# Kernel tuning notes

Hardware: AMD Instinct MI355X
Metric: run time of the kernel (lower is better)

Reference implementation:

```python
import jax, jax.numpy as jnp
import numpy as np

RES = 128        # 2**base_lod, base_lod=7, num_lod=1
FEAT_DIM = 18


def setup_inputs() -> dict:
    key = jax.random.key(0)
    k1, k2 = jax.random.split(key)
    pts = jax.random.uniform(k1, (4, 524288, 3), dtype=jnp.float32)
    codebook = jax.random.normal(k2, (RES ** 3, FEAT_DIM), dtype=jnp.float32) * 0.01
    transform = jnp.eye(4, dtype=jnp.float32)
    return {"pts": pts, "codebook": codebook, "transform": transform}


def _trilinear(res, codebook, pts):
    # pts: [N,3] in [0,1]; NGLOD-style dense grid trilinear interpolation
    p = pts * (res - 1)
    p0 = jnp.floor(p)
    w = p - p0                                   # [N,3] fractional weights
    i0 = jnp.clip(p0.astype(jnp.int32), 0, res - 1)
    i1 = jnp.clip(i0 + 1, 0, res - 1)
    feats = jnp.zeros((pts.shape[0], codebook.shape[1]), dtype=codebook.dtype)
    for dz in (0, 1):
        iz = (i1 if dz else i0)[:, 2]
        wz = w[:, 2] if dz else 1.0 - w[:, 2]
        for dy in (0, 1):
            iy = (i1 if dy else i0)[:, 1]
            wy = w[:, 1] if dy else 1.0 - w[:, 1]
            for dx in (0, 1):
                ix = (i1 if dx else i0)[:, 0]
                wx = w[:, 0] if dx else 1.0 - w[:, 0]
                idx = ix + iy * res + iz * res * res   # x + y*res + z*res^2
                feats = feats + codebook[idx] * (wx * wy * wz)[:, None]
    return feats


def reference(pts, codebook, transform):
    # flatten 'b h c -> (b h) c'
    p = pts.reshape(-1, 3)
    R_inv = jnp.linalg.inv(transform[:3, :3])
    p = (R_inv @ (p.T - transform[:3, 3:4])).T
    feats = _trilinear(RES, codebook, p)
    # single LOD: cat over lod axis then sum(-1) is identity
    return feats
```

## Files before the change

kernel.cpp:

```cpp
#include <hip/hip_runtime.h>


constexpr int RES  = 128;
constexpr int NBA  = 512;
constexpr int TPM  = 576;
constexpr int PPB  = 64;
constexpr int ROWF = 128 * 18;
constexpr int SUB_CAP = 8160;

constexpr int HIST_CHUNK = 1024;
constexpr int SCAT_CHUNK = 8192;

typedef float vf2 __attribute__((ext_vector_type(2)));
typedef float vf4 __attribute__((ext_vector_type(4)));

struct Xf {
    float m00, m01, m02, m10, m11, m12, m20, m21, m22;
    float tx, ty, tz;
};

__device__ __forceinline__ Xf load_xf(const float* __restrict__ tr) {
    Xf X;
    const float a = tr[0], b = tr[1],  c = tr[2];
    const float d = tr[4], e = tr[5],  g = tr[6];
    const float h = tr[8], i = tr[9],  j = tr[10];
    X.tx = tr[3]; X.ty = tr[7]; X.tz = tr[11];
    const float det = a*(e*j - g*i) - b*(d*j - g*h) + c*(d*i - e*h);
    const float rd  = 1.0f / det;
    X.m00 = (e*j - g*i) * rd; X.m01 = (c*i - b*j) * rd; X.m02 = (b*g - c*e) * rd;
    X.m10 = (g*h - d*j) * rd; X.m11 = (a*j - c*h) * rd; X.m12 = (c*d - a*g) * rd;
    X.m20 = (d*i - e*h) * rd; X.m21 = (b*h - a*i) * rd; X.m22 = (a*e - b*d) * rd;
    return X;
}

__device__ __forceinline__ float qcoord(float m0, float m1, float m2,
                                        float x, float y, float z) {
    return __fmaf_rn(m0, x, __fmaf_rn(m1, y, m2 * z)) * (float)(RES - 1);
}

__device__ __forceinline__ int clamp_idx(float q) {
    return min(max((int)floorf(q), 0), RES - 1);
}

__device__ __forceinline__ int coarse_key(float qy, float qz) {
    return (clamp_idx(qz) << 2) | (clamp_idx(qy) >> 5);
}

__global__ __launch_bounds__(256)
void k_zero(unsigned* __restrict__ histA) {
    const int i = blockIdx.x * 256 + threadIdx.x;
    if (i < NBA) histA[i] = 0u;
}

__global__ __launch_bounds__(256)
void k_histA(const float* __restrict__ pts, const float* __restrict__ tr,
             unsigned* __restrict__ histA, int npts)
{
    __shared__ unsigned sh[NBA];
    const int t = threadIdx.x;
    for (int b = t; b < NBA; b += 256) sh[b] = 0u;
    __syncthreads();
    const Xf X = load_xf(tr);
    const int base = blockIdx.x * HIST_CHUNK;
    #pragma unroll
    for (int i = 0; i < HIST_CHUNK / 256; ++i) {
        const int p = base + t + i * 256;
        if (p < npts) {
            const float x = pts[p*3 + 0] - X.tx;
            const float y = pts[p*3 + 1] - X.ty;
            const float z = pts[p*3 + 2] - X.tz;
            const float qy = qcoord(X.m10, X.m11, X.m12, x, y, z);
            const float qz = qcoord(X.m20, X.m21, X.m22, x, y, z);
            atomicAdd(&sh[coarse_key(qy, qz)], 1u);
        }
    }
    __syncthreads();
    for (int b = t; b < NBA; b += 256) {
        const unsigned c = sh[b];
        if (c) atomicAdd(&histA[b], c);
    }
}

__global__ __launch_bounds__(NBA)
void k_scanA(const unsigned* __restrict__ histA,
             unsigned* __restrict__ baseA, unsigned* __restrict__ cursorA)
{
    __shared__ unsigned s[NBA];
    const int t = threadIdx.x;
    const unsigned my = histA[t];
    s[t] = my;
    __syncthreads();
    for (int off = 1; off < NBA; off <<= 1) {
        const unsigned v = (t >= off) ? s[t - off] : 0u;
        __syncthreads();
        s[t] += v;
        __syncthreads();
    }
    baseA[t]   = s[t] - my;
    cursorA[t] = s[t] - my;
}

__global__ __launch_bounds__(256)
void k_scatA(const float* __restrict__ pts, const float* __restrict__ tr,
             unsigned* __restrict__ cursorA, vf4* __restrict__ rec, int npts)
{
    __shared__ unsigned shist[NBA], sbase[NBA], scur[NBA];
    const int t = threadIdx.x;
    for (int b = t; b < NBA; b += 256) { shist[b] = 0u; scur[b] = 0u; }
    __syncthreads();
    const Xf X = load_xf(tr);
    const int base = blockIdx.x * SCAT_CHUNK;
    #pragma unroll
    for (int i = 0; i < SCAT_CHUNK / 256; ++i) {
        const int p = base + t + i * 256;
        if (p < npts) {
            const float x = pts[p*3 + 0] - X.tx;
            const float y = pts[p*3 + 1] - X.ty;
            const float z = pts[p*3 + 2] - X.tz;
            const float qy = qcoord(X.m10, X.m11, X.m12, x, y, z);
            const float qz = qcoord(X.m20, X.m21, X.m22, x, y, z);
            atomicAdd(&shist[coarse_key(qy, qz)], 1u);
        }
    }
    __syncthreads();
    for (int b = t; b < NBA; b += 256)
        sbase[b] = shist[b] ? atomicAdd(&cursorA[b], shist[b]) : 0u;
    __syncthreads();
    #pragma unroll
    for (int i = 0; i < SCAT_CHUNK / 256; ++i) {
        const int p = base + t + i * 256;
        if (p < npts) {
            const float x = pts[p*3 + 0] - X.tx;
            const float y = pts[p*3 + 1] - X.ty;
            const float z = pts[p*3 + 2] - X.tz;
            const float qx = qcoord(X.m00, X.m01, X.m02, x, y, z);
            const float qy = qcoord(X.m10, X.m11, X.m12, x, y, z);
            const float qz = qcoord(X.m20, X.m21, X.m22, x, y, z);
            const int bn = coarse_key(qy, qz);
            const unsigned r = atomicAdd(&scur[bn], 1u);
            unsigned pos = sbase[bn] + r;
            if (pos >= (unsigned)npts) pos = (unsigned)npts - 1u;
            vf4 v; v.x = qx; v.y = qy; v.z = qz; v.w = __int_as_float(p);
            rec[pos] = v;
        }
    }
}

__global__ __launch_bounds__(1024)
void k_subsort(vf4* __restrict__ rec, const unsigned* __restrict__ histA,
               const unsigned* __restrict__ baseA, unsigned* __restrict__ histF)
{
    const int cbn = blockIdx.x;
    const int t = threadIdx.x;
    const unsigned n = histA[cbn];
    const unsigned b0 = baseA[cbn];
    const int iz0 = cbn >> 2;
    const int ybase = (cbn & 3) << 5;
    const int bf = (iz0 << 7) | ybase;

    if (n == 0u) { if (t < 32) histF[bf + t] = 0u; return; }
    if (n > (unsigned)SUB_CAP) {
        if (t < 32) histF[bf + t] = (t == 0) ? (n | 0x80000000u) : 0u;
        return;
    }

    __shared__ vf4 c[SUB_CAP];
    __shared__ unsigned h[32], cur[32];
    if (t < 32) h[t] = 0u;
    __syncthreads();

    for (unsigned i = t; i < n; i += 1024) {
        const vf4 v = rec[b0 + i];
        c[i] = v;
        const int key = min(max(clamp_idx(v.y) - ybase, 0), 31);
        atomicAdd(&h[key], 1u);
    }
    __syncthreads();
    if (t == 0) {
        unsigned run = 0u;
        for (int k = 0; k < 32; ++k) { cur[k] = run; run += h[k]; }
    }
    __syncthreads();
    for (unsigned i = t; i < n; i += 1024) {
        const vf4 v = c[i];
        const int key = min(max(clamp_idx(v.y) - ybase, 0), 31);
        const unsigned pos = atomicAdd(&cur[key], 1u);
        rec[b0 + pos] = v;
    }
    if (t < 32) histF[bf + t] = h[t];
}

__global__ __launch_bounds__(TPM)
void k_main5(const vf4* __restrict__ rec, const unsigned* __restrict__ histF,
             const unsigned* __restrict__ baseA, const float* __restrict__ cbk,
             float* __restrict__ out)
{
    const int blk = blockIdx.x;
    const int iz0 = blk >> 2;
    const int ybase = (blk & 3) << 5;
    const int t = threadIdx.x;
    const int pl = t / 9;
    const int f  = t - pl * 9;

    __shared__ float sld[4][2][ROWF];

    const unsigned bs = baseA[blk];
    const unsigned nj0raw = histF[(iz0 << 7) | ybase];

    auto stage = [&](int yn) {
        const int yc = min(yn, RES - 1);
        const int s  = yn & 3;
        #pragma unroll
        for (int zz = 0; zz < 2; ++zz) {
            const int zc = min(iz0 + zz, RES - 1);
            const vf2* __restrict__ src =
                reinterpret_cast<const vf2*>(cbk + (size_t)((zc << 14) | (yc << 7)) * 18);
            vf2* dst = reinterpret_cast<vf2*>(&sld[s][zz][0]);
            dst[t]       = src[t];
            dst[t + TPM] = src[t + TPM];
        }
    };

    if (nj0raw & 0x80000000u) {
        const unsigned n = nj0raw & 0x7fffffffu;
        for (unsigned off = 0; off < n; off += PPB) {
            const unsigned pi = off + (unsigned)pl;
            if (pi < n) {
                const vf4 r = rec[bs + pi];
                const float qx = r.x, qy = r.y, qz = r.z;
                const int idx = __float_as_int(r.w);
                const float fx = floorf(qx), fy = floorf(qy), fz = floorf(qz);
                const float wx1 = qx - fx, wy1 = qy - fy, wz1 = qz - fz;
                const float wx0 = 1.0f - wx1, wy0 = 1.0f - wy1, wz0 = 1.0f - wz1;
                const int ix0 = clamp_idx(qx), ix1 = min(ix0 + 1, RES - 1);
                const int iy0 = clamp_idx(qy), iy1 = min(iy0 + 1, RES - 1);
                const int izp = clamp_idx(qz), iz1 = min(izp + 1, RES - 1);
                vf2 v[8]; float w[8];
                #pragma unroll
                for (int k = 0; k < 8; ++k) {
                    const int dx = k & 1, dy = (k >> 1) & 1, dz = k >> 2;
                    const int ro = (dx ? ix1 : ix0) + ((dy ? iy1 : iy0) << 7)
                                 + ((dz ? iz1 : izp) << 14);
                    v[k] = *reinterpret_cast<const vf2*>(cbk + (size_t)ro * 18 + 2 * f);
                    w[k] = (dx ? wx1 : wx0) * (dy ? wy1 : wy0) * (dz ? wz1 : wz0);
                }
                float ax = 0.0f, ay = 0.0f;
                #pragma unroll
                for (int k = 0; k < 8; ++k) { ax += v[k].x * w[k]; ay += v[k].y * w[k]; }
                vf2 o; o.x = ax; o.y = ay;
                __builtin_nontemporal_store(o,
                    reinterpret_cast<vf2*>(out + (size_t)idx * 18 + 2 * f));
            }
        }
        return;
    }

    stage(ybase);
    stage(ybase + 1);
    unsigned cur = bs;
    __syncthreads();

    for (int j = 0; j < 32; ++j) {
        const int iy0 = ybase + j;
        const unsigned nj = histF[(iz0 << 7) | iy0];
        if (j < 31) stage(iy0 + 2);

        const int sy0 = iy0 & 3, sy1 = (iy0 + 1) & 3;
        for (unsigned off = 0; off < nj; off += PPB) {
            const unsigned pi = off + (unsigned)pl;
            if (pi < nj) {
                const vf4 r = __builtin_nontemporal_load(&rec[cur + pi]);
                const float qx = r.x, qy = r.y, qz = r.z;
                const int idx = __float_as_int(r.w);
                const float fx = floorf(qx), fy = floorf(qy), fz = floorf(qz);
                const float wx1 = qx - fx, wy1 = qy - fy, wz1 = qz - fz;
                const float wx0 = 1.0f - wx1, wy0 = 1.0f - wy1, wz0 = 1.0f - wz1;
                const int ix0 = clamp_idx(qx), ix1 = min(ix0 + 1, RES - 1);
                const int x0 = ix0 * 18 + 2 * f, x1 = ix1 * 18 + 2 * f;
                vf2 v[8]; float w[8];
                #pragma unroll
                for (int k = 0; k < 8; ++k) {
                    const int dx = k & 1, dy = (k >> 1) & 1, dz = k >> 2;
                    const float* base_ = &sld[dy ? sy1 : sy0][dz][0];
                    v[k] = *reinterpret_cast<const vf2*>(&base_[dx ? x1 : x0]);
                    w[k] = (dx ? wx1 : wx0) * (dy ? wy1 : wy0) * (dz ? wz1 : wz0);
                }
                float ax = 0.0f, ay = 0.0f;
                #pragma unroll
                for (int k = 0; k < 8; ++k) { ax += v[k].x * w[k]; ay += v[k].y * w[k]; }
                vf2 o; o.x = ax; o.y = ay;
                __builtin_nontemporal_store(o,
                    reinterpret_cast<vf2*>(out + (size_t)idx * 18 + 2 * f));
            }
        }
        cur += nj;
        __syncthreads();
    }
}

__global__ __launch_bounds__(TPM)
void dense_grid_trilerp(const float* __restrict__ pts,
                        const float* __restrict__ cb,
                        const float* __restrict__ tr,
                        float* __restrict__ out,
                        int npts)
{
    __shared__ float spts[PPB * 3];
    if (threadIdx.x < PPB * 3) {
        int g = blockIdx.x * (PPB * 3) + threadIdx.x;
        spts[threadIdx.x] = (g < npts * 3) ? __builtin_nontemporal_load(&pts[g]) : 0.0f;
    }
    __syncthreads();

    const int pl = threadIdx.x / 9;
    const int f  = threadIdx.x - pl * 9;
    const int p  = blockIdx.x * PPB + pl;
    if (p >= npts) return;

    const Xf X = load_xf(tr);
    const float x = spts[pl*3 + 0] - X.tx;
    const float y = spts[pl*3 + 1] - X.ty;
    const float z = spts[pl*3 + 2] - X.tz;
    const float qx = qcoord(X.m00, X.m01, X.m02, x, y, z);
    const float qy = qcoord(X.m10, X.m11, X.m12, x, y, z);
    const float qz = qcoord(X.m20, X.m21, X.m22, x, y, z);

    const float fx = floorf(qx), fy = floorf(qy), fz = floorf(qz);
    const float wx1 = qx - fx, wy1 = qy - fy, wz1 = qz - fz;
    const float wx0 = 1.0f - wx1, wy0 = 1.0f - wy1, wz0 = 1.0f - wz1;
    const int ix0 = clamp_idx(qx); const int ix1 = min(ix0 + 1, RES - 1);
    const int iy0 = clamp_idx(qy); const int iy1 = min(iy0 + 1, RES - 1);
    const int iz0 = clamp_idx(qz); const int iz1 = min(iz0 + 1, RES - 1);

    int   ro[8];
    float w[8];
    #pragma unroll
    for (int k = 0; k < 8; ++k) {
        const int dx = k & 1, dy = (k >> 1) & 1, dz = k >> 2;
        ro[k] = (dx ? ix1 : ix0) + ((dy ? iy1 : iy0) << 7) + ((dz ? iz1 : iz0) << 14);
        w[k]  = (dx ? wx1 : wx0) * (dy ? wy1 : wy0) * (dz ? wz1 : wz0);
    }

    const float* cbf = cb + 2 * f;
    vf2 v[8];
    #pragma unroll
    for (int k = 0; k < 8; ++k)
        v[k] = *reinterpret_cast<const vf2*>(cbf + ro[k] * 18);

    float ax = 0.0f, ay = 0.0f;
    #pragma unroll
    for (int k = 0; k < 8; ++k) { ax += v[k].x * w[k]; ay += v[k].y * w[k]; }

    vf2 o; o.x = ax; o.y = ay;
    __builtin_nontemporal_store(o, reinterpret_cast<vf2*>(out + p * 18 + 2 * f));
}

extern "C" void kernel_launch(void* const* d_in, const int* in_sizes, int n_in,
                              void* d_out, int out_size, void* d_ws, size_t ws_size,
                              hipStream_t stream) {
    const float* pts = (const float*)d_in[0];
    const float* cb  = (const float*)d_in[1];
    const float* tr  = (const float*)d_in[2];
    float* out = (float*)d_out;

    const int npts = in_sizes[0] / 3;

    const size_t meta = (size_t)(NBA * 3 + 16384) * sizeof(unsigned);
    const size_t need = meta + (size_t)npts * 16;
    if (d_ws == nullptr || ws_size < need || npts <= 0) {
        const int blocks = (npts + PPB - 1) / PPB;
        dense_grid_trilerp<<<blocks, TPM, 0, stream>>>(pts, cb, tr, out, npts);
        return;
    }

    unsigned* histA   = (unsigned*)d_ws;
    unsigned* baseA   = histA + NBA;
    unsigned* cursorA = baseA + NBA;
    unsigned* histF   = cursorA + NBA;
    vf4* rec = (vf4*)((char*)d_ws + meta);

    k_zero<<<(NBA + 255) / 256, 256, 0, stream>>>(histA);
    k_histA<<<(npts + HIST_CHUNK - 1) / HIST_CHUNK, 256, 0, stream>>>(pts, tr, histA, npts);
    k_scanA<<<1, NBA, 0, stream>>>(histA, baseA, cursorA);
    k_scatA<<<(npts + SCAT_CHUNK - 1) / SCAT_CHUNK, 256, 0, stream>>>(pts, tr, cursorA, rec, npts);
    k_subsort<<<NBA, 1024, 0, stream>>>(rec, histA, baseA, histF);
    k_main5<<<NBA, TPM, 0, stream>>>(rec, histF, baseA, cb, out);
}
```

Before: 506.6 us.

## Replace LDS-staged slab gather with L2-friendly sorted-point gather and XCD block remap

The per-slab main kernel, which staged codebook rows into LDS and walked y-rows serially, is replaced by a flat kernel with one workgroup per 64 sorted points. Each workgroup gathers the eight corners straight from global memory. The subsort now orders points by (y, x/16) inside each coarse bucket to improve cache locality. Workgroup IDs are remapped so consecutive sorted chunks land on the same XCD and share its L2. Alongside this, the scatter chunk size is doubled and its unroll pragma removed, trading LDS reuse for much higher parallelism and relying on L2 hits.

Result: slower. 523.7 us (+3.4%).

```diff
diff --git a/kernel.cpp b/kernel.cpp
--- a/kernel.cpp
+++ b/kernel.cpp
@@ -5,11 +5,10 @@
 constexpr int NBA  = 512;
 constexpr int TPM  = 576;
 constexpr int PPB  = 64;
-constexpr int ROWF = 128 * 18;
 constexpr int SUB_CAP = 8160;
 
 constexpr int HIST_CHUNK = 1024;
-constexpr int SCAT_CHUNK = 8192;
+constexpr int SCAT_CHUNK = 16384;
 
 typedef float vf2 __attribute__((ext_vector_type(2)));
 typedef float vf4 __attribute__((ext_vector_type(4)));
@@ -110,7 +109,6 @@
     __syncthreads();
     const Xf X = load_xf(tr);
     const int base = blockIdx.x * SCAT_CHUNK;
-    #pragma unroll
     for (int i = 0; i < SCAT_CHUNK / 256; ++i) {
         const int p = base + t + i * 256;
         if (p < npts) {
@@ -126,7 +124,6 @@
     for (int b = t; b < NBA; b += 256)
         sbase[b] = shist[b] ? atomicAdd(&cursorA[b], shist[b]) : 0u;
     __syncthreads();
-    #pragma unroll
     for (int i = 0; i < SCAT_CHUNK / 256; ++i) {
         const int p = base + t + i * 256;
         if (p < npts) {
@@ -148,154 +145,98 @@
 
 __global__ __launch_bounds__(1024)
 void k_subsort(vf4* __restrict__ rec, const unsigned* __restrict__ histA,
-               const unsigned* __restrict__ baseA, unsigned* __restrict__ histF)
+               const unsigned* __restrict__ baseA)
 {
     const int cbn = blockIdx.x;
     const int t = threadIdx.x;
     const unsigned n = histA[cbn];
     const unsigned b0 = baseA[cbn];
-    const int iz0 = cbn >> 2;
     const int ybase = (cbn & 3) << 5;
-    const int bf = (iz0 << 7) | ybase;
-
-    if (n == 0u) { if (t < 32) histF[bf + t] = 0u; return; }
-    if (n > (unsigned)SUB_CAP) {
-        if (t < 32) histF[bf + t] = (t == 0) ? (n | 0x80000000u) : 0u;
-        return;
-    }
+
+    if (n == 0u || n > (unsigned)SUB_CAP) return;
 
     __shared__ vf4 c[SUB_CAP];
-    __shared__ unsigned h[32], cur[32];
-    if (t < 32) h[t] = 0u;
+    __shared__ unsigned h[256], cur[256];
+    for (int k = t; k < 256; k += 1024) h[k] = 0u;
     __syncthreads();
 
     for (unsigned i = t; i < n; i += 1024) {
         const vf4 v = rec[b0 + i];
         c[i] = v;
-        const int key = min(max(clamp_idx(v.y) - ybase, 0), 31);
-        atomicAdd(&h[key], 1u);
+        const int ky = min(max(clamp_idx(v.y) - ybase, 0), 31);
+        const int kx = clamp_idx(v.x) >> 4;
+        atomicAdd(&h[(ky << 3) | kx], 1u);
     }
     __syncthreads();
     if (t == 0) {
         unsigned run = 0u;
-        for (int k = 0; k < 32; ++k) { cur[k] = run; run += h[k]; }
+        for (int k = 0; k < 256; ++k) { cur[k] = run; run += h[k]; }
     }
     __syncthreads();
     for (unsigned i = t; i < n; i += 1024) {
         const vf4 v = c[i];
-        const int key = min(max(clamp_idx(v.y) - ybase, 0), 31);
-        const unsigned pos = atomicAdd(&cur[key], 1u);
+        const int ky = min(max(clamp_idx(v.y) - ybase, 0), 31);
+        const int kx = clamp_idx(v.x) >> 4;
+        const unsigned pos = atomicAdd(&cur[(ky << 3) | kx], 1u);
         rec[b0 + pos] = v;
     }
-    if (t < 32) histF[bf + t] = h[t];
 }
 
 __global__ __launch_bounds__(TPM)
-void k_main5(const vf4* __restrict__ rec, const unsigned* __restrict__ histF,
-             const unsigned* __restrict__ baseA, const float* __restrict__ cbk,
-             float* __restrict__ out)
-{
-    const int blk = blockIdx.x;
-    const int iz0 = blk >> 2;
-    const int ybase = (blk & 3) << 5;
-    const int t = threadIdx.x;
+void k_main6(const vf4* __restrict__ rec, const float* __restrict__ cb,
+             float* __restrict__ out, int npts, int nwg)
+{
+    const int bid = blockIdx.x;
+    const int q = nwg >> 3, r = nwg & 7;
+    const int xcd = bid & 7, lin = bid >> 3;
+    const int blk = (xcd < r ? xcd * (q + 1) : r * (q + 1) + (xcd - r) * q) + lin;
+
+    __shared__ vf4 srec[PPB];
+    const int t = threadIdx.x;
+    const int g0 = blk * PPB;
+    if (t < PPB) {
+        const int g = g0 + t;
+        if (g < npts) srec[t] = __builtin_nontemporal_load(&rec[g]);
+    }
+    __syncthreads();
+
     const int pl = t / 9;
     const int f  = t - pl * 9;
-
-    __shared__ float sld[4][2][ROWF];
-
-    const unsigned bs = baseA[blk];
-    const unsigned nj0raw = histF[(iz0 << 7) | ybase];
-
-    auto stage = [&](int yn) {
-        const int yc = min(yn, RES - 1);
-        const int s  = yn & 3;
-        #pragma unroll
-        for (int zz = 0; zz < 2; ++zz) {
-            const int zc = min(iz0 + zz, RES - 1);
-            const vf2* __restrict__ src =
-                reinterpret_cast<const vf2*>(cbk + (size_t)((zc << 14) | (yc << 7)) * 18);
-            vf2* dst = reinterpret_cast<vf2*>(&sld[s][zz][0]);
-            dst[t]       = src[t];
-            dst[t + TPM] = src[t + TPM];
-        }
-    };
-
-    if (nj0raw & 0x80000000u) {
-        const unsigned n = nj0raw & 0x7fffffffu;
-        for (unsigned off = 0; off < n; off += PPB) {
-            const unsigned pi = off + (unsigned)pl;
-            if (pi < n) {
-                const vf4 r = rec[bs + pi];
-                const float qx = r.x, qy = r.y, qz = r.z;
-                const int idx = __float_as_int(r.w);
-                const float fx = floorf(qx), fy = floorf(qy), fz = floorf(qz);
-                const float wx1 = qx - fx, wy1 = qy - fy, wz1 = qz - fz;
-                const float wx0 = 1.0f - wx1, wy0 = 1.0f - wy1, wz0 = 1.0f - wz1;
-                const int ix0 = clamp_idx(qx), ix1 = min(ix0 + 1, RES - 1);
-                const int iy0 = clamp_idx(qy), iy1 = min(iy0 + 1, RES - 1);
-                const int izp = clamp_idx(qz), iz1 = min(izp + 1, RES - 1);
-                vf2 v[8]; float w[8];
-                #pragma unroll
-                for (int k = 0; k < 8; ++k) {
-                    const int dx = k & 1, dy = (k >> 1) & 1, dz = k >> 2;
-                    const int ro = (dx ? ix1 : ix0) + ((dy ? iy1 : iy0) << 7)
-                                 + ((dz ? iz1 : izp) << 14);
-                    v[k] = *reinterpret_cast<const vf2*>(cbk + (size_t)ro * 18 + 2 * f);
-                    w[k] = (dx ? wx1 : wx0) * (dy ? wy1 : wy0) * (dz ? wz1 : wz0);
-                }
-                float ax = 0.0f, ay = 0.0f;
-                #pragma unroll
-                for (int k = 0; k < 8; ++k) { ax += v[k].x * w[k]; ay += v[k].y * w[k]; }
-                vf2 o; o.x = ax; o.y = ay;
-                __builtin_nontemporal_store(o,
-                    reinterpret_cast<vf2*>(out + (size_t)idx * 18 + 2 * f));
-            }
-        }
-        return;
-    }
-
-    stage(ybase);
-    stage(ybase + 1);
-    unsigned cur = bs;
-    __syncthreads();
-
-    for (int j = 0; j < 32; ++j) {
-        const int iy0 = ybase + j;
-        const unsigned nj = histF[(iz0 << 7) | iy0];
-        if (j < 31) stage(iy0 + 2);
-
-        const int sy0 = iy0 & 3, sy1 = (iy0 + 1) & 3;
-        for (unsigned off = 0; off < nj; off += PPB) {
-            const unsigned pi = off + (unsigned)pl;
-            if (pi < nj) {
-                const vf4 r = __builtin_nontemporal_load(&rec[cur + pi]);
-                const float qx = r.x, qy = r.y, qz = r.z;
-                const int idx = __float_as_int(r.w);
-                const float fx = floorf(qx), fy = floorf(qy), fz = floorf(qz);
-                const float wx1 = qx - fx, wy1 = qy - fy, wz1 = qz - fz;
-                const float wx0 = 1.0f - wx1, wy0 = 1.0f - wy1, wz0 = 1.0f - wz1;
-                const int ix0 = clamp_idx(qx), ix1 = min(ix0 + 1, RES - 1);
-                const int x0 = ix0 * 18 + 2 * f, x1 = ix1 * 18 + 2 * f;
-                vf2 v[8]; float w[8];
-                #pragma unroll
-                for (int k = 0; k < 8; ++k) {
-                    const int dx = k & 1, dy = (k >> 1) & 1, dz = k >> 2;
-                    const float* base_ = &sld[dy ? sy1 : sy0][dz][0];
-                    v[k] = *reinterpret_cast<const vf2*>(&base_[dx ? x1 : x0]);
-                    w[k] = (dx ? wx1 : wx0) * (dy ? wy1 : wy0) * (dz ? wz1 : wz0);
-                }
-                float ax = 0.0f, ay = 0.0f;
-                #pragma unroll
-                for (int k = 0; k < 8; ++k) { ax += v[k].x * w[k]; ay += v[k].y * w[k]; }
-                vf2 o; o.x = ax; o.y = ay;
-                __builtin_nontemporal_store(o,
-                    reinterpret_cast<vf2*>(out + (size_t)idx * 18 + 2 * f));
-            }
-        }
-        cur += nj;
-        __syncthreads();
-    }
+    const int p  = g0 + pl;
+    if (p >= npts) return;
+
+    const vf4 rr = srec[pl];
+    const float qx = rr.x, qy = rr.y, qz = rr.z;
+    const int idx = __float_as_int(rr.w);
+
+    const float fx = floorf(qx), fy = floorf(qy), fz = floorf(qz);
+    const float wx1 = qx - fx, wy1 = qy - fy, wz1 = qz - fz;
+    const float wx0 = 1.0f - wx1, wy0 = 1.0f - wy1, wz0 = 1.0f - wz1;
+    const int ix0 = clamp_idx(qx); const int ix1 = min(ix0 + 1, RES - 1);
+    const int iy0 = clamp_idx(qy); const int iy1 = min(iy0 + 1, RES - 1);
+    const int iz0 = clamp_idx(qz); const int iz1 = min(iz0 + 1, RES - 1);
+
+    int   ro[8];
+    float w[8];
+    #pragma unroll
+    for (int k = 0; k < 8; ++k) {
+        const int dx = k & 1, dy = (k >> 1) & 1, dz = k >> 2;
+        ro[k] = (dx ? ix1 : ix0) + ((dy ? iy1 : iy0) << 7) + ((dz ? iz1 : iz0) << 14);
+        w[k]  = (dx ? wx1 : wx0) * (dy ? wy1 : wy0) * (dz ? wz1 : wz0);
+    }
+
+    const float* cbf = cb + 2 * f;
+    vf2 v[8];
+    #pragma unroll
+    for (int k = 0; k < 8; ++k)
+        v[k] = *reinterpret_cast<const vf2*>(cbf + (size_t)ro[k] * 18);
+
+    float ax = 0.0f, ay = 0.0f;
+    #pragma unroll
+    for (int k = 0; k < 8; ++k) { ax += v[k].x * w[k]; ay += v[k].y * w[k]; }
+
+    vf2 o; o.x = ax; o.y = ay;
+    __builtin_nontemporal_store(o, reinterpret_cast<vf2*>(out + (size_t)idx * 18 + 2 * f));
 }
 
 __global__ __launch_bounds__(TPM)
@@ -345,7 +286,7 @@
     vf2 v[8];
     #pragma unroll
     for (int k = 0; k < 8; ++k)
-        v[k] = *reinterpret_cast<const vf2*>(cbf + ro[k] * 18);
+        v[k] = *reinterpret_cast<const vf2*>(cbf + (size_t)ro[k] * 18);
 
     float ax = 0.0f, ay = 0.0f;
     #pragma unroll
@@ -365,7 +306,7 @@
 
     const int npts = in_sizes[0] / 3;
 
-    const size_t meta = (size_t)(NBA * 3 + 16384) * sizeof(unsigned);
+    const size_t meta = (size_t)(NBA * 3) * sizeof(unsigned);
     const size_t need = meta + (size_t)npts * 16;
     if (d_ws == nullptr || ws_size < need || npts <= 0) {
         const int blocks = (npts + PPB - 1) / PPB;
@@ -376,13 +317,13 @@
     unsigned* histA   = (unsigned*)d_ws;
     unsigned* baseA   = histA + NBA;
     unsigned* cursorA = baseA + NBA;
-    unsigned* histF   = cursorA + NBA;
     vf4* rec = (vf4*)((char*)d_ws + meta);
 
+    const int nwg = (npts + PPB - 1) / PPB;
     k_zero<<<(NBA + 255) / 256, 256, 0, stream>>>(histA);
     k_histA<<<(npts + HIST_CHUNK - 1) / HIST_CHUNK, 256, 0, stream>>>(pts, tr, histA, npts);
     k_scanA<<<1, NBA, 0, stream>>>(histA, baseA, cursorA);
     k_scatA<<<(npts + SCAT_CHUNK - 1) / SCAT_CHUNK, 256, 0, stream>>>(pts, tr, cursorA, rec, npts);
-    k_subsort<<<NBA, 1024, 0, stream>>>(rec, histA, baseA, histF);
-    k_main5<<<NBA, TPM, 0, stream>>>(rec, histF, baseA, cb, out);
-}
+    k_subsort<<<NBA, 1024, 0, stream>>>(rec, histA, baseA);
+    k_main6<<<nwg, TPM, 0, stream>>>(rec, cb, out, npts, nwg);
+}
```
